# Kernel tuning notes

Hardware: AMD Instinct MI355X
Metric: run time of the kernel (lower is better)

## Reference

```python
import jax, jax.numpy as jnp
import numpy as np

H0, H1, NL, B, S = 2048, 1024, 8, 2, 2048

def _linear(x, w, b):
    return jnp.einsum('bsd,od->bso', x, w) + b

def setup_inputs() -> dict:
    key = jax.random.key(0)
    ks = jax.random.split(key, 32)
    d = {
        'z':    jax.random.normal(ks[0], (B, S, H0), jnp.float32),
        'act0': jax.random.normal(ks[1], (B, S, H0), jnp.float32),
        'act1': jax.random.normal(ks[2], (B, S, H0), jnp.float32),
        'attmask': jax.random.randint(ks[3], (B, S), 0, 2, jnp.int32),
        'dproj_w': jax.random.normal(ks[4], (H1, H0), jnp.float32) * 0.02,
        'dproj_b': jnp.zeros((H1,), jnp.float32),
        'uproj_w': jax.random.normal(ks[5], (H0, H1), jnp.float32) * 0.02,
        'uproj_b': jnp.zeros((H0,), jnp.float32),
        'wq_w': jax.random.normal(ks[6], (NL, H1, H1), jnp.float32) * 0.02,
        'wq_b': jnp.zeros((NL, H1), jnp.float32),
        'wk_w': jax.random.normal(ks[7], (NL, H1, H1), jnp.float32) * 0.02,
        'wk_b': jnp.zeros((NL, H1), jnp.float32),
        'wv_w': jax.random.normal(ks[8], (NL, H1, H1), jnp.float32) * 0.02,
        'wv_b': jnp.zeros((NL, H1), jnp.float32),
        'mlp1_w': jax.random.normal(ks[9], (NL, 4 * H1, H1), jnp.float32) * 0.02,
        'mlp1_b': jnp.zeros((NL, 4 * H1), jnp.float32),
        'mlp2_w': jax.random.normal(ks[10], (NL, H1, 4 * H1), jnp.float32) * 0.02,
        'mlp2_b': jnp.zeros((NL, H1), jnp.float32),
    }
    return d

def _ladder_fwd(z, act0, act1, attmask, dproj_w, dproj_b, uproj_w, uproj_b,
                wq_w, wq_b, wk_w, wk_b, wv_w, wv_b,
                mlp1_w, mlp1_b, mlp2_w, mlp2_b):
    seq = z.shape[1]
    scale = 1.0 / jnp.sqrt(jnp.float32(H1))
    causal = jnp.tril(jnp.ones((seq, seq), bool))  # [S,S]
    pad = (attmask != 0)[:, None, :]               # [B,1,S] key padding mask
    neg = jnp.float32(-1e9)

    def ladsatt(i, x):
        Q = _linear(x, wq_w[i], wq_b[i])
        K = _linear(x, wk_w[i], wk_b[i])
        V = _linear(x, wv_w[i], wv_b[i])
        scores = jnp.einsum('bqd,bkd->bqk', Q, K) * scale
        scores = jnp.where(causal[None], scores, neg)
        scores = jnp.where(pad, scores, neg)
        w = jax.nn.softmax(scores, axis=-1)
        return jnp.einsum('bqk,bkd->bqd', w, V)

    def mlp(i, x):
        h = jax.nn.relu(_linear(x, mlp1_w[i], mlp1_b[i]))
        return _linear(h, mlp2_w[i], mlp2_b[i])

    rs = _linear(act0, dproj_w, dproj_b)
    rs = rs + ladsatt(0, rs)
    rs = rs + mlp(0, rs)
    rs = rs + _linear(act1, dproj_w, dproj_b)
    rs = rs + ladsatt(1, rs)
    rs = rs + mlp(1, rs)
    for i in range(2, NL):
        rs = rs + ladsatt(i, rs)
        rs = rs + mlp(i, rs)
    return _linear(rs, uproj_w, uproj_b) + z

def reference(z, act0, act1, attmask, dproj_w, dproj_b, uproj_w, uproj_b,
              wq_w, wq_b, wk_w, wk_b, wv_w, wv_b,
              mlp1_w, mlp1_b, mlp2_w, mlp2_b):
    return _ladder_fwd(z, act0, act1, attmask, dproj_w, dproj_b, uproj_w, uproj_b,
                       wq_w, wq_b, wk_w, wk_b, wv_w, wv_b,
                       mlp1_w, mlp1_b, mlp2_w, mlp2_b)
```

## Files before the change

kernel.cpp:

```cpp
#include <hip/hip_runtime.h>
#include <cstdint>


typedef unsigned short u16;
typedef __attribute__((ext_vector_type(8))) __bf16 bf16x8;
typedef __attribute__((ext_vector_type(4))) float f32x4;

#define DI __device__ __forceinline__

constexpr int BB = 2, SSQ = 2048, HH0 = 2048, HH1 = 1024, NLAY = 8, HH4 = 4096;
constexpr int MM = BB * SSQ;

DI float bf2f(u16 h) {
  union { uint32_t u; float f; } x; x.u = ((uint32_t)h) << 16; return x.f;
}
DI u16 f2bf(float f) {
  union { float f; uint32_t u; } x; x.f = f;
  uint32_t u = x.u;
  return (u16)((u + 0x7fffu + ((u >> 16) & 1u)) >> 16);
}

enum {
  FB_BIAS = 1, FB_RES = 2, FB_RELU = 4, FB_F32 = 8, FB_SPLIT = 16,
  FB_CSKIP = 32, FB_CKLOOP = 64
};

template <int F, int KSP>
__global__ __launch_bounds__(256) void gemm_split(
    const u16* __restrict__ Ah, const u16* __restrict__ Al, long sAz, int lda,
    const u16* __restrict__ Bh, const u16* __restrict__ Bl, long sBz, int ldb,
    const float* __restrict__ bias, const float* __restrict__ resF,
    float* Cf, u16* Ch, u16* Cl, long sCz, int ldc, int K, long pstride) {
  int gx = gridDim.x, gy = gridDim.y, gz = gridDim.z;
  long o = blockIdx.x + (long)gx * (blockIdx.y + (long)gy * blockIdx.z);
  long nwg = (long)gx * gy * gz;
  long cq = nwg >> 3, cr = nwg & 7;
  long xcd = o & 7, cidx = o >> 3;
  long sl = (xcd < cr ? xcd * (cq + 1) : cr * (cq + 1) + (xcd - cr) * cq) + cidx;
  int bx = (int)(sl % gx);
  long tt = sl / gx;
  int by = (int)(tt % gy);
  int bzf = (int)(tt / gy);
  int NB = gz / KSP;
  int bz = bzf % NB;
  int ks = bzf / NB;

  if ((F & FB_CSKIP) && bx > by) return;

  __shared__ __align__(16) u16 Sbuf[2][4][128 * 32];

  int tid = threadIdx.x;
  int lane = tid & 63;
  int wave = tid >> 6;
  int wr = (wave >> 1) << 6;
  int wc = (wave & 1) << 6;
  int lrow = lane & 15;
  int kg = lane >> 4;
  int kc8 = (kg ^ ((lrow >> 1) & 3)) << 3;

  const u16* Abh = Ah + (long)bz * sAz + ((long)(by << 7)) * lda;
  const u16* Abl = Al + (long)bz * sAz + ((long)(by << 7)) * lda;
  const u16* Bbh = Bh + (long)bz * sBz + ((long)(bx << 7)) * ldb;
  const u16* Bbl = Bl + (long)bz * sBz + ((long)(bx << 7)) * ldb;

  int nKtot = (F & FB_CKLOOP) ? ((by + 1) << 2) : (K >> 5);
  int kbeg = (KSP > 1) ? (ks * nKtot) / KSP : 0;
  int kend = (KSP > 1) ? ((ks + 1) * nKtot) / KSP : nKtot;

  f32x4 acc[4][4] = {};

  auto STAGE = [&](int buf, int kt) {
    int k0 = kt << 5;
#pragma unroll
    for (int it = 0; it < 2; ++it) {
      int sidx = (it << 8) + tid;
      int r = sidx >> 2;
      int jsw = (sidx & 3) ^ ((r >> 1) & 3);
      long goff = (long)r * lda + (k0 + (jsw << 3));
      long gofB = (long)r * ldb + (k0 + (jsw << 3));
      int loff = sidx << 3;
      __builtin_amdgcn_global_load_lds(
          (__attribute__((address_space(1))) void*)(Abh + goff),
          (__attribute__((address_space(3))) void*)(&Sbuf[buf][0][loff]), 16, 0, 0);
      __builtin_amdgcn_global_load_lds(
          (__attribute__((address_space(1))) void*)(Abl + goff),
          (__attribute__((address_space(3))) void*)(&Sbuf[buf][1][loff]), 16, 0, 0);
      __builtin_amdgcn_global_load_lds(
          (__attribute__((address_space(1))) void*)(Bbh + gofB),
          (__attribute__((address_space(3))) void*)(&Sbuf[buf][2][loff]), 16, 0, 0);
      __builtin_amdgcn_global_load_lds(
          (__attribute__((address_space(1))) void*)(Bbl + gofB),
          (__attribute__((address_space(3))) void*)(&Sbuf[buf][3][loff]), 16, 0, 0);
    }
  };

  auto COMPUTE = [&](int buf) {
    bf16x8 afh[4], bfh[4], bfl[4];
#pragma unroll
    for (int mi = 0; mi < 4; ++mi)
      afh[mi] = *(const bf16x8*)&Sbuf[buf][0][((wr + (mi << 4) + lrow) << 5) + kc8];
#pragma unroll
    for (int ni = 0; ni < 4; ++ni) {
      bfh[ni] = *(const bf16x8*)&Sbuf[buf][2][((wc + (ni << 4) + lrow) << 5) + kc8];
      bfl[ni] = *(const bf16x8*)&Sbuf[buf][3][((wc + (ni << 4) + lrow) << 5) + kc8];
    }
#pragma unroll
    for (int mi = 0; mi < 4; ++mi)
#pragma unroll
      for (int ni = 0; ni < 4; ++ni) {
        acc[mi][ni] = __builtin_amdgcn_mfma_f32_16x16x32_bf16(
            afh[mi], bfh[ni], acc[mi][ni], 0, 0, 0);
        acc[mi][ni] = __builtin_amdgcn_mfma_f32_16x16x32_bf16(
            afh[mi], bfl[ni], acc[mi][ni], 0, 0, 0);
      }
    bf16x8 afl[4];
#pragma unroll
    for (int mi = 0; mi < 4; ++mi)
      afl[mi] = *(const bf16x8*)&Sbuf[buf][1][((wr + (mi << 4) + lrow) << 5) + kc8];
#pragma unroll
    for (int mi = 0; mi < 4; ++mi)
#pragma unroll
      for (int ni = 0; ni < 4; ++ni)
        acc[mi][ni] = __builtin_amdgcn_mfma_f32_16x16x32_bf16(
            afl[mi], bfh[ni], acc[mi][ni], 0, 0, 0);
  };

  STAGE(0, kbeg);
  int cur = 0;
  for (int kt = kbeg; kt < kend; ++kt) {
    bool more = (kt + 1 < kend);
    if (more) STAGE(cur ^ 1, kt + 1);
    if (more) asm volatile("s_waitcnt vmcnt(8)" ::: "memory");
    else      asm volatile("s_waitcnt vmcnt(0)" ::: "memory");
    __builtin_amdgcn_s_barrier();
    asm volatile("" ::: "memory");
    COMPUTE(cur);
    asm volatile("" ::: "memory");
    __builtin_amdgcn_s_barrier();
    asm volatile("" ::: "memory");
    cur ^= 1;
  }

  int m0 = (by << 7) + wr + (kg << 2);
  int n0 = (bx << 7) + wc;
#pragma unroll
  for (int mi = 0; mi < 4; ++mi) {
#pragma unroll
    for (int ni = 0; ni < 4; ++ni) {
      int col = n0 + (ni << 4) + lrow;
      float bv = 0.f;
      if ((KSP == 1) && (F & FB_BIAS)) bv = bias[col];
      int rb = m0 + (mi << 4);
#pragma unroll
      for (int r = 0; r < 4; ++r) {
        float v = acc[mi][ni][r];
        long ci = (long)bz * sCz + (long)(rb + r) * ldc + col;
        if constexpr (KSP > 1) {
          Cf[(long)ks * pstride + ci] = v;
        } else {
          v += bv;
          if (F & FB_RELU) v = fmaxf(v, 0.f);
          if (F & FB_RES) v += resF[ci];
          if (F & FB_F32) Cf[ci] = v;
          if (F & FB_SPLIT) {
            u16 h = f2bf(v);
            Ch[ci] = h;
            Cl[ci] = f2bf(v - bf2f(h));
          }
        }
      }
    }
  }
}

template <bool RES>
__global__ void reduce_split(const float* __restrict__ p,
                             const float* __restrict__ bias,
                             float* __restrict__ rs, u16* __restrict__ xh,
                             u16* __restrict__ xl) {
  long i = ((long)blockIdx.x * 256 + threadIdx.x) << 2;
  int col = (int)(i & 1023);
  float4 a = *(const float4*)(p + i);
  float4 b = *(const float4*)(p + i + (long)MM * HH1);
  float4 v;
  v.x = a.x + b.x + bias[col];
  v.y = a.y + b.y + bias[col + 1];
  v.z = a.z + b.z + bias[col + 2];
  v.w = a.w + b.w + bias[col + 3];
  if (RES) {
    float4 r0 = *(const float4*)(rs + i);
    v.x += r0.x; v.y += r0.y; v.z += r0.z; v.w += r0.w;
  }
  *(float4*)(rs + i) = v;
  ushort4 h, l;
  h.x = f2bf(v.x); l.x = f2bf(v.x - bf2f(h.x));
  h.y = f2bf(v.y); l.y = f2bf(v.y - bf2f(h.y));
  h.z = f2bf(v.z); l.z = f2bf(v.z - bf2f(h.z));
  h.w = f2bf(v.w); l.w = f2bf(v.w - bf2f(h.w));
  *(ushort4*)(xh + i) = h;
  *(ushort4*)(xl + i) = l;
}

__global__ void split_kernel(const float* __restrict__ src, u16* __restrict__ hi,
                             u16* __restrict__ lo) {
  long i = ((long)blockIdx.x * 256 + threadIdx.x) << 2;
  float4 v = *(const float4*)(src + i);
  ushort4 h, l;
  h.x = f2bf(v.x); l.x = f2bf(v.x - bf2f(h.x));
  h.y = f2bf(v.y); l.y = f2bf(v.y - bf2f(h.y));
  h.z = f2bf(v.z); l.z = f2bf(v.z - bf2f(h.z));
  h.w = f2bf(v.w); l.w = f2bf(v.w - bf2f(h.w));
  *(ushort4*)(hi + i) = h;
  *(ushort4*)(lo + i) = l;
}

__global__ void concat_bias(const float* __restrict__ qb, const float* __restrict__ kb,
                            const float* __restrict__ vb, float* __restrict__ dst) {
  int j = blockIdx.x * 256 + threadIdx.x;
  float v = (j < 1024) ? qb[j] : ((j < 2048) ? kb[j - 1024] : vb[j - 2048]);
  dst[j] = v;
}

__global__ void deg_kernel(const int* __restrict__ am, int* __restrict__ deg) {
  int i = blockIdx.x * 256 + threadIdx.x;
  int b = i >> 11, q = i & 2047;
  const int* a = am + b * SSQ;
  int any = 0;
  for (int k = 0; k <= q; ++k) any |= (a[k] != 0);
  deg[i] = !any;
}

__global__ void transpose_v2(const u16* __restrict__ Vh, const u16* __restrict__ Vl,
                             int sld, u16* __restrict__ VTh, u16* __restrict__ VTl) {
  __shared__ u16 th[64][68];
  __shared__ u16 tl[64][68];
  int b = blockIdx.z;
  int c0 = blockIdx.x << 6;
  int r0 = blockIdx.y << 6;
  int tr = threadIdx.x >> 4, tc = threadIdx.x & 15;
  long sbase = ((long)(b * SSQ + r0)) * sld + c0;
#pragma unroll
  for (int j = 0; j < 4; ++j) {
    int r = (j << 4) + tr;
    ushort4 uh = *(const ushort4*)(Vh + sbase + (long)r * sld + (tc << 2));
    ushort4 ul = *(const ushort4*)(Vl + sbase + (long)r * sld + (tc << 2));
    th[r][(tc << 2) + 0] = uh.x; th[r][(tc << 2) + 1] = uh.y;
    th[r][(tc << 2) + 2] = uh.z; th[r][(tc << 2) + 3] = uh.w;
    tl[r][(tc << 2) + 0] = ul.x; tl[r][(tc << 2) + 1] = ul.y;
    tl[r][(tc << 2) + 2] = ul.z; tl[r][(tc << 2) + 3] = ul.w;
  }
  __syncthreads();
  long dbase = ((long)b * HH1 + c0) * SSQ + r0;
#pragma unroll
  for (int j = 0; j < 4; ++j) {
    int c = (j << 4) + tr;
    ushort4 uh, ul;
    uh.x = th[(tc << 2) + 0][c]; uh.y = th[(tc << 2) + 1][c];
    uh.z = th[(tc << 2) + 2][c]; uh.w = th[(tc << 2) + 3][c];
    ul.x = tl[(tc << 2) + 0][c]; ul.y = tl[(tc << 2) + 1][c];
    ul.z = tl[(tc << 2) + 2][c]; ul.w = tl[(tc << 2) + 3][c];
    *(ushort4*)(VTh + dbase + (long)c * SSQ + (tc << 2)) = uh;
    *(ushort4*)(VTl + dbase + (long)c * SSQ + (tc << 2)) = ul;
  }
}

__global__ void colmean_partial(const u16* __restrict__ Vh, const u16* __restrict__ Vl,
                                int ld, float* __restrict__ part) {
  int n = blockIdx.x * 256 + threadIdx.x;
  int b = blockIdx.y, kc = blockIdx.z;
  long base = ((long)(b * SSQ + kc * 256)) * ld + n;
  float s = 0.f;
  for (int k = 0; k < 256; ++k) {
    long o = base + (long)k * ld;
    s += bf2f(Vh[o]) + bf2f(Vl[o]);
  }
  part[((kc * BB) + b) * HH1 + n] = s;
}
__global__ void colmean_final(const float* __restrict__ part, float* __restrict__ mV) {
  int i = blockIdx.x * 256 + threadIdx.x;
  int b = i >> 10, n = i & 1023;
  float s = 0.f;
  for (int kc = 0; kc < 8; ++kc) s += part[((kc * BB) + b) * HH1 + n];
  mV[i] = s * (1.f / (float)SSQ);
}

__global__ void softmax_kernel(const float* __restrict__ sc, u16* __restrict__ Ph,
                               u16* __restrict__ Pl, const int* __restrict__ am,
                               const int* __restrict__ deg) {
  int q = blockIdx.x, b = blockIdx.y;
  int tid = threadIdx.x;
  long rowoff = ((long)b * SSQ + q) * SSQ;
  int qt_end = ((q >> 7) + 1) << 7;
  if (deg[b * SSQ + q]) {
    for (int k = tid; k < qt_end; k += 256) { Ph[rowoff + k] = 0; Pl[rowoff + k] = 0; }
    return;
  }
  const int* a = am + b * SSQ;
  const float scale = 0.03125f;
  constexpr long PSTR = (long)BB * SSQ * SSQ;
  __shared__ float rowbuf[2048];
  __shared__ float sred[8];
  int w = tid >> 6, ln = tid & 63;

  for (int k = tid; k < qt_end; k += 256)
    rowbuf[k] = sc[rowoff + k] + sc[rowoff + k + PSTR];
  __syncthreads();

  float m = -1e30f;
  for (int k = tid; k <= q; k += 256)
    if (a[k]) m = fmaxf(m, rowbuf[k]);
#pragma unroll
  for (int o = 32; o; o >>= 1) m = fmaxf(m, __shfl_xor(m, o));
  if (!ln) sred[w] = m;
  __syncthreads();
  float M = fmaxf(fmaxf(sred[0], sred[1]), fmaxf(sred[2], sred[3]));

  float s = 0.f;
  for (int k = tid; k <= q; k += 256)
    if (a[k]) s += expf((rowbuf[k] - M) * scale);
#pragma unroll
  for (int o = 32; o; o >>= 1) s += __shfl_xor(s, o);
  if (!ln) sred[4 + w] = s;
  __syncthreads();
  float Ssum = sred[4] + sred[5] + sred[6] + sred[7];
  float inv = 1.f / Ssum;

  for (int k = tid; k < qt_end; k += 256) {
    float p = 0.f;
    if (k <= q && a[k]) p = expf((rowbuf[k] - M) * scale) * inv;
    u16 h = f2bf(p);
    Ph[rowoff + k] = h;
    Pl[rowoff + k] = f2bf(p - bf2f(h));
  }
}

__global__ void attn_post(float* __restrict__ rs, const float* __restrict__ pv,
                          u16* __restrict__ xh, u16* __restrict__ xl,
                          const int* __restrict__ deg, const float* __restrict__ mV) {
  long t = (long)blockIdx.x * 256 + threadIdx.x;
  long i = t << 2;
  int row = (int)(i >> 10);
  int col = (int)(i & 1023);
  int b = row >> 11;
  constexpr long PSTR = (long)BB * SSQ * HH1;
  float4 v = *(const float4*)(rs + i);
  float4 a = *(const float4*)(pv + i);
  float4 c = *(const float4*)(pv + i + PSTR);
  v.x += a.x + c.x; v.y += a.y + c.y; v.z += a.z + c.z; v.w += a.w + c.w;
  if (deg[row]) {
    const float* m = mV + (b << 10) + col;
    v.x += m[0]; v.y += m[1]; v.z += m[2]; v.w += m[3];
  }
  *(float4*)(rs + i) = v;
  ushort4 h, l;
  h.x = f2bf(v.x); l.x = f2bf(v.x - bf2f(h.x));
  h.y = f2bf(v.y); l.y = f2bf(v.y - bf2f(h.y));
  h.z = f2bf(v.z); l.z = f2bf(v.z - bf2f(h.z));
  h.w = f2bf(v.w); l.w = f2bf(v.w - bf2f(h.w));
  *(ushort4*)(xh + i) = h;
  *(ushort4*)(xl + i) = l;
}

constexpr size_t MB = 1u << 20;
constexpr size_t OFF_RS    = 0;
constexpr size_t OFF_XH    = 16 * MB;
constexpr size_t OFF_XL    = 24 * MB;
constexpr size_t OFF_QKVH  = 32 * MB;
constexpr size_t OFF_QKVL  = 56 * MB;
constexpr size_t OFF_PH    = 32 * MB;
constexpr size_t OFF_PL    = 48 * MB;
constexpr size_t OFF_RED   = 32 * MB;
constexpr size_t OFF_VTH   = 80 * MB;
constexpr size_t OFF_VTL   = 88 * MB;
constexpr size_t OFF_SC    = 96 * MB;
constexpr size_t OFF_ACTH  = 96 * MB;
constexpr size_t OFF_ACTL  = 112 * MB;
constexpr size_t OFF_HH    = 96 * MB;
constexpr size_t OFF_HL    = 128 * MB;
constexpr size_t OFF_PVP   = 128 * MB;
constexpr size_t OFF_DPWH  = 160 * MB;
constexpr size_t OFF_DPWL  = 164 * MB;
constexpr size_t OFF_UPWH  = 168 * MB;
constexpr size_t OFF_UPWL  = 172 * MB;
constexpr size_t OFF_WQKVH = 176 * MB;
constexpr size_t OFF_WQKVL = 182 * MB;
constexpr size_t OFF_M1H   = 188 * MB;
constexpr size_t OFF_M1L   = 196 * MB;
constexpr size_t OFF_M2H   = 204 * MB;
constexpr size_t OFF_M2L   = 212 * MB;
constexpr size_t OFF_QKVB  = 220 * MB;
constexpr size_t OFF_MV    = OFF_QKVB + 16 * 1024;
constexpr size_t OFF_PART  = OFF_MV + 16 * 1024;
constexpr size_t OFF_DEG   = OFF_PART + 128 * 1024;

extern "C" void kernel_launch(void* const* d_in, const int* in_sizes, int n_in,
                              void* d_out, int out_size, void* d_ws, size_t ws_size,
                              hipStream_t stream) {
  (void)in_sizes; (void)n_in; (void)out_size; (void)ws_size;

  const float* z    = (const float*)d_in[0];
  const float* act0 = (const float*)d_in[1];
  const float* act1 = (const float*)d_in[2];
  const int* amask  = (const int*)d_in[3];
  const float* dpw  = (const float*)d_in[4];
  const float* dpb  = (const float*)d_in[5];
  const float* upw  = (const float*)d_in[6];
  const float* upb  = (const float*)d_in[7];
  const float* wqw  = (const float*)d_in[8];
  const float* wqb  = (const float*)d_in[9];
  const float* wkw  = (const float*)d_in[10];
  const float* wkb  = (const float*)d_in[11];
  const float* wvw  = (const float*)d_in[12];
  const float* wvb  = (const float*)d_in[13];
  const float* m1w  = (const float*)d_in[14];
  const float* m1b  = (const float*)d_in[15];
  const float* m2w  = (const float*)d_in[16];
  const float* m2b  = (const float*)d_in[17];

  char* ws = (char*)d_ws;
  float* rs    = (float*)(ws + OFF_RS);
  u16* xh      = (u16*)(ws + OFF_XH);    u16* xl    = (u16*)(ws + OFF_XL);
  u16* qkvh    = (u16*)(ws + OFF_QKVH);  u16* qkvl  = (u16*)(ws + OFF_QKVL);
  u16* Ph      = (u16*)(ws + OFF_PH);    u16* Pl    = (u16*)(ws + OFF_PL);
  float* redp  = (float*)(ws + OFF_RED);
  u16* VTh     = (u16*)(ws + OFF_VTH);   u16* VTl   = (u16*)(ws + OFF_VTL);
  float* scb   = (float*)(ws + OFF_SC);
  u16* acth    = (u16*)(ws + OFF_ACTH);  u16* actl  = (u16*)(ws + OFF_ACTL);
  u16* hh      = (u16*)(ws + OFF_HH);    u16* hl    = (u16*)(ws + OFF_HL);
  float* pvp   = (float*)(ws + OFF_PVP);
  u16* dpwh    = (u16*)(ws + OFF_DPWH);  u16* dpwl  = (u16*)(ws + OFF_DPWL);
  u16* upwh    = (u16*)(ws + OFF_UPWH);  u16* upwl  = (u16*)(ws + OFF_UPWL);
  u16* wqkvh   = (u16*)(ws + OFF_WQKVH); u16* wqkvl = (u16*)(ws + OFF_WQKVL);
  u16* m1h     = (u16*)(ws + OFF_M1H);   u16* m1l   = (u16*)(ws + OFF_M1L);
  u16* m2h     = (u16*)(ws + OFF_M2H);   u16* m2l   = (u16*)(ws + OFF_M2L);
  float* qkvb  = (float*)(ws + OFF_QKVB);
  float* mV    = (float*)(ws + OFF_MV);
  float* part  = (float*)(ws + OFF_PART);
  int* deg     = (int*)(ws + OFF_DEG);

  deg_kernel<<<dim3((BB * SSQ) / 256), 256, 0, stream>>>(amask, deg);
  split_kernel<<<dim3((HH1 * HH0) / 1024), 256, 0, stream>>>(dpw, dpwh, dpwl);
  split_kernel<<<dim3((HH0 * HH1) / 1024), 256, 0, stream>>>(upw, upwh, upwl);

  split_kernel<<<dim3((MM * HH0) / 1024), 256, 0, stream>>>(act0, acth, actl);
  gemm_split<0, 2><<<dim3(HH1 / 128, MM / 128, 2), 256, 0, stream>>>(
      acth, actl, 0, HH0, dpwh, dpwl, 0, HH0, nullptr, nullptr,
      redp, nullptr, nullptr, 0, HH1, HH0, (long)MM * HH1);
  reduce_split<false><<<dim3(MM * HH1 / 1024), 256, 0, stream>>>(redp, dpb, rs, xh, xl);

  for (int i = 0; i < NLAY; ++i) {
    split_kernel<<<dim3((HH1 * HH1) / 1024), 256, 0, stream>>>(
        wqw + (size_t)i * HH1 * HH1, wqkvh, wqkvl);
    split_kernel<<<dim3((HH1 * HH1) / 1024), 256, 0, stream>>>(
        wkw + (size_t)i * HH1 * HH1, wqkvh + HH1 * HH1, wqkvl + HH1 * HH1);
    split_kernel<<<dim3((HH1 * HH1) / 1024), 256, 0, stream>>>(
        wvw + (size_t)i * HH1 * HH1, wqkvh + 2 * HH1 * HH1, wqkvl + 2 * HH1 * HH1);
    concat_bias<<<dim3(12), 256, 0, stream>>>(wqb + i * HH1, wkb + i * HH1,
                                              wvb + i * HH1, qkvb);
    split_kernel<<<dim3((HH4 * HH1) / 1024), 256, 0, stream>>>(
        m1w + (size_t)i * HH4 * HH1, m1h, m1l);
    split_kernel<<<dim3((HH1 * HH4) / 1024), 256, 0, stream>>>(
        m2w + (size_t)i * HH1 * HH4, m2h, m2l);

    if (i == 1) {
      split_kernel<<<dim3((MM * HH0) / 1024), 256, 0, stream>>>(act1, acth, actl);
      gemm_split<0, 2><<<dim3(HH1 / 128, MM / 128, 2), 256, 0, stream>>>(
          acth, actl, 0, HH0, dpwh, dpwl, 0, HH0, nullptr, nullptr,
          redp, nullptr, nullptr, 0, HH1, HH0, (long)MM * HH1);
      reduce_split<true><<<dim3(MM * HH1 / 1024), 256, 0, stream>>>(redp, dpb, rs, xh, xl);
    }

    gemm_split<FB_BIAS | FB_SPLIT, 1><<<dim3(3072 / 128, MM / 128, 1), 256, 0, stream>>>(
        xh, xl, 0, HH1, wqkvh, wqkvl, 0, HH1, qkvb, nullptr,
        nullptr, qkvh, qkvl, 0, 3072, HH1, 0);

    transpose_v2<<<dim3(HH1 / 64, SSQ / 64, BB), 256, 0, stream>>>(
        qkvh + 2048, qkvl + 2048, 3072, VTh, VTl);
    colmean_partial<<<dim3(HH1 / 256, BB, 8), 256, 0, stream>>>(
        qkvh + 2048, qkvl + 2048, 3072, part);
    colmean_final<<<dim3((BB * HH1) / 256), 256, 0, stream>>>(part, mV);

    gemm_split<FB_CSKIP, 2><<<dim3(SSQ / 128, SSQ / 128, BB * 2), 256, 0, stream>>>(
        qkvh, qkvl, (long)SSQ * 3072, 3072, qkvh + 1024, qkvl + 1024,
        (long)SSQ * 3072, 3072, nullptr, nullptr,
        scb, nullptr, nullptr, (long)SSQ * SSQ, SSQ, HH1, (long)BB * SSQ * SSQ);

    softmax_kernel<<<dim3(SSQ, BB), 256, 0, stream>>>(scb, Ph, Pl, amask, deg);

    gemm_split<FB_CKLOOP, 2><<<dim3(HH1 / 128, SSQ / 128, BB * 2), 256, 0, stream>>>(
        Ph, Pl, (long)SSQ * SSQ, SSQ, VTh, VTl, (long)HH1 * SSQ, SSQ, nullptr, nullptr,
        pvp, nullptr, nullptr, (long)SSQ * HH1, HH1, SSQ, (long)BB * SSQ * HH1);

    attn_post<<<dim3((MM * HH1 / 4) / 256), 256, 0, stream>>>(rs, pvp, xh, xl, deg, mV);

    gemm_split<FB_BIAS | FB_RELU | FB_SPLIT, 1>
        <<<dim3(HH4 / 128, MM / 128, 1), 256, 0, stream>>>(
        xh, xl, 0, HH1, m1h, m1l, 0, HH1, m1b + i * HH4, nullptr,
        nullptr, hh, hl, 0, HH4, HH1, 0);
    gemm_split<0, 2><<<dim3(HH1 / 128, MM / 128, 2), 256, 0, stream>>>(
        hh, hl, 0, HH4, m2h, m2l, 0, HH4, nullptr, nullptr,
        redp, nullptr, nullptr, 0, HH1, HH4, (long)MM * HH1);
    reduce_split<true><<<dim3(MM * HH1 / 1024), 256, 0, stream>>>(
        redp, m2b + i * HH1, rs, xh, xl);
  }

  gemm_split<FB_BIAS | FB_RES | FB_F32, 1>
      <<<dim3(HH0 / 128, MM / 128, 1), 256, 0, stream>>>(
      xh, xl, 0, HH1, upwh, upwl, 0, HH1, upb, z,
      (float*)d_out, nullptr, nullptr, 0, HH0, HH1, 0);
}
```

Baseline: 4.053 ms.

## Add 256x256 direct-to-LDS GEMM kernel for MLP and down-projection

Adds a new split-bf16 GEMM kernel with a 256x256 block tile and 512 threads. It uses global_load_lds async copies into double-buffered, swizzled LDS and remaps workgroups so consecutive tiles land on the same XCD. The kernel replaces the 128x128 GEMMs for the MLP up/down projections and the input down-projections, with those reductions moving from split-K 2 to split-K 4. The larger tiles are meant to raise arithmetic intensity and hide load latency. The cost is 128KB of LDS per block, which limits occupancy, plus twice the partial-sum buffer traffic, which needs a workspace large enough for four partitions.

```diff
diff --git a/kernel.cpp b/kernel.cpp
--- a/kernel.cpp
+++ b/kernel.cpp
@@ -173,20 +173,157 @@
   }
 }
 
-template <bool RES>
+template <int F, int KSP>
+__global__ __launch_bounds__(512, 2) void gemm_big(
+    const u16* __restrict__ Ah, const u16* __restrict__ Al, int lda,
+    const u16* __restrict__ Bh, const u16* __restrict__ Bl, int ldb,
+    const float* __restrict__ bias,
+    float* Cf, u16* Ch, u16* Cl, int ldc, int K, long pstride) {
+  int gx = gridDim.x, gy = gridDim.y, gz = gridDim.z;
+  long o = blockIdx.x + (long)gx * (blockIdx.y + (long)gy * blockIdx.z);
+  long nwg = (long)gx * gy * gz;
+  long cq = nwg >> 3, cr = nwg & 7;
+  long xcd = o & 7, cidx = o >> 3;
+  long sl = (xcd < cr ? xcd * (cq + 1) : cr * (cq + 1) + (xcd - cr) * cq) + cidx;
+  int bx = (int)(sl % gx);
+  long tt = sl / gx;
+  int by = (int)(tt % gy);
+  int ks = (int)(tt / gy);
+
+  __shared__ __align__(16) u16 Sbuf[2][4][256 * 32];
+
+  int tid = threadIdx.x;
+  int lane = tid & 63;
+  int wave = tid >> 6;
+  int wm = (wave >> 2) << 7;
+  int wn = (wave & 3) << 6;
+  int lrow = lane & 15;
+  int kg = lane >> 4;
+  int kc8 = (kg ^ ((lrow >> 1) & 3)) << 3;
+
+  const u16* Abh = Ah + ((long)(by << 8)) * lda;
+  const u16* Abl = Al + ((long)(by << 8)) * lda;
+  const u16* Bbh = Bh + ((long)(bx << 8)) * ldb;
+  const u16* Bbl = Bl + ((long)(bx << 8)) * ldb;
+
+  int nKtot = K >> 5;
+  int kbeg = (KSP > 1) ? (ks * nKtot) / KSP : 0;
+  int kend = (KSP > 1) ? ((ks + 1) * nKtot) / KSP : nKtot;
+
+  f32x4 acc[8][4] = {};
+
+  auto STAGE = [&](int buf, int kt) {
+    int k0 = kt << 5;
+#pragma unroll
+    for (int it = 0; it < 2; ++it) {
+      int sidx = (it << 9) + tid;
+      int r = sidx >> 2;
+      int jsw = (sidx & 3) ^ ((r >> 1) & 3);
+      long goff = (long)r * lda + (k0 + (jsw << 3));
+      long gofB = (long)r * ldb + (k0 + (jsw << 3));
+      int loff = sidx << 3;
+      __builtin_amdgcn_global_load_lds(
+          (__attribute__((address_space(1))) void*)(Abh + goff),
+          (__attribute__((address_space(3))) void*)(&Sbuf[buf][0][loff]), 16, 0, 0);
+      __builtin_amdgcn_global_load_lds(
+          (__attribute__((address_space(1))) void*)(Abl + goff),
+          (__attribute__((address_space(3))) void*)(&Sbuf[buf][1][loff]), 16, 0, 0);
+      __builtin_amdgcn_global_load_lds(
+          (__attribute__((address_space(1))) void*)(Bbh + gofB),
+          (__attribute__((address_space(3))) void*)(&Sbuf[buf][2][loff]), 16, 0, 0);
+      __builtin_amdgcn_global_load_lds(
+          (__attribute__((address_space(1))) void*)(Bbl + gofB),
+          (__attribute__((address_space(3))) void*)(&Sbuf[buf][3][loff]), 16, 0, 0);
+    }
+  };
+
+  auto COMPUTE = [&](int buf) {
+    bf16x8 bfh[4], bfl[4];
+#pragma unroll
+    for (int ni = 0; ni < 4; ++ni) {
+      int brow = wn + (ni << 4) + lrow;
+      bfh[ni] = *(const bf16x8*)&Sbuf[buf][2][(brow << 5) + kc8];
+      bfl[ni] = *(const bf16x8*)&Sbuf[buf][3][(brow << 5) + kc8];
+    }
+#pragma unroll
+    for (int mi = 0; mi < 8; ++mi) {
+      int arow = wm + (mi << 4) + lrow;
+      bf16x8 ah = *(const bf16x8*)&Sbuf[buf][0][(arow << 5) + kc8];
+      bf16x8 al = *(const bf16x8*)&Sbuf[buf][1][(arow << 5) + kc8];
+#pragma unroll
+      for (int ni = 0; ni < 4; ++ni) {
+        acc[mi][ni] = __builtin_amdgcn_mfma_f32_16x16x32_bf16(
+            ah, bfh[ni], acc[mi][ni], 0, 0, 0);
+        acc[mi][ni] = __builtin_amdgcn_mfma_f32_16x16x32_bf16(
+            ah, bfl[ni], acc[mi][ni], 0, 0, 0);
+        acc[mi][ni] = __builtin_amdgcn_mfma_f32_16x16x32_bf16(
+            al, bfh[ni], acc[mi][ni], 0, 0, 0);
+      }
+    }
+  };
+
+  STAGE(0, kbeg);
+  int cur = 0;
+  for (int kt = kbeg; kt < kend; ++kt) {
+    bool more = (kt + 1 < kend);
+    if (more) STAGE(cur ^ 1, kt + 1);
+    if (more) asm volatile("s_waitcnt vmcnt(8)" ::: "memory");
+    else      asm volatile("s_waitcnt vmcnt(0)" ::: "memory");
+    __builtin_amdgcn_s_barrier();
+    asm volatile("" ::: "memory");
+    COMPUTE(cur);
+    asm volatile("" ::: "memory");
+    __builtin_amdgcn_s_barrier();
+    asm volatile("" ::: "memory");
+    cur ^= 1;
+  }
+
+  int m0 = (by << 8) + wm + (kg << 2);
+  int n0 = (bx << 8) + wn;
+#pragma unroll
+  for (int mi = 0; mi < 8; ++mi) {
+#pragma unroll
+    for (int ni = 0; ni < 4; ++ni) {
+      int col = n0 + (ni << 4) + lrow;
+      float bv = 0.f;
+      if ((KSP == 1) && (F & FB_BIAS)) bv = bias[col];
+      int rb = m0 + (mi << 4);
+#pragma unroll
+      for (int r = 0; r < 4; ++r) {
+        float v = acc[mi][ni][r];
+        long ci = (long)(rb + r) * ldc + col;
+        if constexpr (KSP > 1) {
+          Cf[(long)ks * pstride + ci] = v;
+        } else {
+          v += bv;
+          if (F & FB_RELU) v = fmaxf(v, 0.f);
+          if (F & FB_F32) Cf[ci] = v;
+          if (F & FB_SPLIT) {
+            u16 h = f2bf(v);
+            Ch[ci] = h;
+            Cl[ci] = f2bf(v - bf2f(h));
+          }
+        }
+      }
+    }
+  }
+}
+
+template <int KSP, bool RES>
 __global__ void reduce_split(const float* __restrict__ p,
                              const float* __restrict__ bias,
                              float* __restrict__ rs, u16* __restrict__ xh,
                              u16* __restrict__ xl) {
   long i = ((long)blockIdx.x * 256 + threadIdx.x) << 2;
   int col = (int)(i & 1023);
-  float4 a = *(const float4*)(p + i);
-  float4 b = *(const float4*)(p + i + (long)MM * HH1);
+  constexpr long PSTR = (long)MM * HH1;
   float4 v;
-  v.x = a.x + b.x + bias[col];
-  v.y = a.y + b.y + bias[col + 1];
-  v.z = a.z + b.z + bias[col + 2];
-  v.w = a.w + b.w + bias[col + 3];
+  v.x = bias[col]; v.y = bias[col + 1]; v.z = bias[col + 2]; v.w = bias[col + 3];
+#pragma unroll
+  for (int j = 0; j < KSP; ++j) {
+    float4 a = *(const float4*)(p + i + j * PSTR);
+    v.x += a.x; v.y += a.y; v.z += a.z; v.w += a.w;
+  }
   if (RES) {
     float4 r0 = *(const float4*)(rs + i);
     v.x += r0.x; v.y += r0.y; v.z += r0.z; v.w += r0.w;
@@ -438,15 +575,18 @@
   float* part  = (float*)(ws + OFF_PART);
   int* deg     = (int*)(ws + OFF_DEG);
 
+  constexpr long RPSTR = (long)MM * HH1;
+
   deg_kernel<<<dim3((BB * SSQ) / 256), 256, 0, stream>>>(amask, deg);
   split_kernel<<<dim3((HH1 * HH0) / 1024), 256, 0, stream>>>(dpw, dpwh, dpwl);
   split_kernel<<<dim3((HH0 * HH1) / 1024), 256, 0, stream>>>(upw, upwh, upwl);
 
   split_kernel<<<dim3((MM * HH0) / 1024), 256, 0, stream>>>(act0, acth, actl);
-  gemm_split<0, 2><<<dim3(HH1 / 128, MM / 128, 2), 256, 0, stream>>>(
-      acth, actl, 0, HH0, dpwh, dpwl, 0, HH0, nullptr, nullptr,
-      redp, nullptr, nullptr, 0, HH1, HH0, (long)MM * HH1);
-  reduce_split<false><<<dim3(MM * HH1 / 1024), 256, 0, stream>>>(redp, dpb, rs, xh, xl);
+  gemm_big<0, 4><<<dim3(HH1 / 256, MM / 256, 4), 512, 0, stream>>>(
+      acth, actl, HH0, dpwh, dpwl, HH0, nullptr,
+      redp, nullptr, nullptr, HH1, HH0, RPSTR);
+  reduce_split<4, false><<<dim3(MM * HH1 / 1024), 256, 0, stream>>>(
+      redp, dpb, rs, xh, xl);
 
   for (int i = 0; i < NLAY; ++i) {
     split_kernel<<<dim3((HH1 * HH1) / 1024), 256, 0, stream>>>(
@@ -464,10 +604,11 @@
 
     if (i == 1) {
       split_kernel<<<dim3((MM * HH0) / 1024), 256, 0, stream>>>(act1, acth, actl);
-      gemm_split<0, 2><<<dim3(HH1 / 128, MM / 128, 2), 256, 0, stream>>>(
-          acth, actl, 0, HH0, dpwh, dpwl, 0, HH0, nullptr, nullptr,
-          redp, nullptr, nullptr, 0, HH1, HH0, (long)MM * HH1);
-      reduce_split<true><<<dim3(MM * HH1 / 1024), 256, 0, stream>>>(redp, dpb, rs, xh, xl);
+      gemm_big<0, 4><<<dim3(HH1 / 256, MM / 256, 4), 512, 0, stream>>>(
+          acth, actl, HH0, dpwh, dpwl, HH0, nullptr,
+          redp, nullptr, nullptr, HH1, HH0, RPSTR);
+      reduce_split<4, true><<<dim3(MM * HH1 / 1024), 256, 0, stream>>>(
+          redp, dpb, rs, xh, xl);
     }
 
     gemm_split<FB_BIAS | FB_SPLIT, 1><<<dim3(3072 / 128, MM / 128, 1), 256, 0, stream>>>(
@@ -493,14 +634,14 @@
 
     attn_post<<<dim3((MM * HH1 / 4) / 256), 256, 0, stream>>>(rs, pvp, xh, xl, deg, mV);
 
-    gemm_split<FB_BIAS | FB_RELU | FB_SPLIT, 1>
-        <<<dim3(HH4 / 128, MM / 128, 1), 256, 0, stream>>>(
-        xh, xl, 0, HH1, m1h, m1l, 0, HH1, m1b + i * HH4, nullptr,
-        nullptr, hh, hl, 0, HH4, HH1, 0);
-    gemm_split<0, 2><<<dim3(HH1 / 128, MM / 128, 2), 256, 0, stream>>>(
-        hh, hl, 0, HH4, m2h, m2l, 0, HH4, nullptr, nullptr,
-        redp, nullptr, nullptr, 0, HH1, HH4, (long)MM * HH1);
-    reduce_split<true><<<dim3(MM * HH1 / 1024), 256, 0, stream>>>(
+    gemm_big<FB_BIAS | FB_RELU | FB_SPLIT, 1>
+        <<<dim3(HH4 / 256, MM / 256, 1), 512, 0, stream>>>(
+        xh, xl, HH1, m1h, m1l, HH1, m1b + i * HH4,
+        nullptr, hh, hl, HH4, HH1, 0);
+    gemm_big<0, 4><<<dim3(HH1 / 256, MM / 256, 4), 512, 0, stream>>>(
+        hh, hl, HH4, m2h, m2l, HH4, nullptr,
+        redp, nullptr, nullptr, HH1, HH4, RPSTR);
+    reduce_split<4, true><<<dim3(MM * HH1 / 1024), 256, 0, stream>>>(
         redp, m2b + i * HH1, rs, xh, xl);
   }
 
```

After: 3.922 ms. 3.2% less time.
